# Kernel tuning notes

Measured on AMD Instinct MI355X. Metric: run time of the kernel, lower is better.

## Reference

```python
import jax, jax.numpy as jnp
import numpy as np
from jax import lax

# Conv3d(in_dim, in_dim, kernel=(1,3,3), padding=(0,1,1)) == per-time-slice 3x3 conv mixing channels

def _conv3d(x, w, b):
    # x: [B, C, T, W, H], w: [O, I, 1, 3, 3], b: [O]
    y = lax.conv_general_dilated(
        x, w,
        window_strides=(1, 1, 1),
        padding=[(0, 0), (1, 1), (1, 1)],
        dimension_numbers=("NCDHW", "OIDHW", "NCDHW"),
    )
    return y + b[None, :, None, None, None]


def setup_inputs() -> dict:
    key = jax.random.key(0)
    ks = jax.random.split(key, 8)
    B, C, T, W, H = 8, 64, 16, 64, 64
    fan = C * 1 * 3 * 3
    bound = 1.0 / np.sqrt(fan)  # torch Conv3d default init range
    x = jax.random.normal(ks[0], (B, C, T, W, H), dtype=jnp.float32)
    wq = jax.random.uniform(ks[1], (C, C, 1, 3, 3), jnp.float32, -bound, bound)
    wk = jax.random.uniform(ks[2], (C, C, 1, 3, 3), jnp.float32, -bound, bound)
    wv = jax.random.uniform(ks[3], (C, C, 1, 3, 3), jnp.float32, -bound, bound)
    bq = jax.random.uniform(ks[4], (C,), jnp.float32, -bound, bound)
    bk = jax.random.uniform(ks[5], (C,), jnp.float32, -bound, bound)
    bv = jax.random.uniform(ks[6], (C,), jnp.float32, -bound, bound)
    # torch init is gamma=0 (identity output); use nonzero so reference exercises the full path
    gamma = jax.random.normal(ks[7], (1,), dtype=jnp.float32) * 0.1
    return {"x": x, "wq": wq, "wk": wk, "wv": wv,
            "bq": bq, "bk": bk, "bv": bv, "gamma": gamma}


def reference(x, wq, wk, wv, bq, bk, bv, gamma):
    B, C, T, W, H = x.shape
    WH = W * H
    q = _conv3d(x, wq, bq).reshape(B, C, T, WH)
    k = _conv3d(x, wk, bk).reshape(B, C, T, WH)
    v = _conv3d(x, wv, bv).reshape(B, C, T, WH)
    # Original: (q[...,:,None] @ k[...,None,:]) @ v[...,:,None]  -> rank-1 energy, no softmax.
    # Exact reassociation: out_i = q_i * sum_j(k_j * v_j), avoiding the [WH, WH] matrix.
    s = jnp.sum(k * v, axis=-1, keepdims=True)  # [B, C, T, 1]
    out = (q * s).reshape(B, C, T, W, H)
    return gamma[0] * out + x
```

## Files before the change

kernel.cpp:

```cpp
#include <hip/hip_runtime.h>
#include <hip/hip_bf16.h>
#include <stdint.h>

typedef __attribute__((ext_vector_type(8))) short bf16x8;
typedef __attribute__((ext_vector_type(4))) float f32x4v;
typedef __attribute__((ext_vector_type(16))) float f32x16;

#define CH_STRIDE 65536
#define ROW_B 8448
#define SLICE_B 557568

__device__ __forceinline__ uint16_t f2bf(float f) {
  uint32_t u = __builtin_bit_cast(uint32_t, f);
  u = (u + 0x7FFFu + ((u >> 16) & 1u)) >> 16;
  return (uint16_t)u;
}
__device__ __forceinline__ float bf2f(uint32_t b) {
  return __builtin_bit_cast(float, b << 16);
}
__device__ __forceinline__ uint16_t cvt_bf(float f) {
  return __builtin_bit_cast(uint16_t, __float2bfloat16(f));
}

#define MFMA32(a, b, c) __builtin_amdgcn_mfma_f32_32x32x16_bf16(a, b, c, 0, 0, 0)
#define LGKM0 asm volatile("s_waitcnt lgkmcnt(0)" ::: "memory")
#define BAR __builtin_amdgcn_s_barrier()
#define SCHED0 __builtin_amdgcn_sched_barrier(0)

#define LDSX6  (6 * 8 * 66 * 16)
#define LDSX10 (10 * 8 * 66 * 16)

__device__ __forceinline__ bf16x8 ldx(const uint8_t* ldsx, int row, int oct, int ci) {
  return *(const bf16x8*)(ldsx + (uint32_t)((row * 8 + oct) * 66 + ci) * 16u);
}

__device__ __forceinline__ bf16x8 ldw_kv(const uint8_t* ldsw, int oct, int rowloc) {
  return *(const bf16x8*)(ldsw + (uint32_t)(oct * 128 + rowloc) * 16u);
}
__device__ __forceinline__ bf16x8 ldw_q(const uint8_t* ldsw, int oct, int row) {
  return *(const bf16x8*)(ldsw + (uint32_t)(oct * 64 + row) * 16u);
}
__device__ __forceinline__ void ldw_g_q(bf16x8* r, const uint16_t* wq, int tap, int tid) {
  #pragma unroll
  for (int k = 0; k < 2; ++k)
    r[k] = *(const bf16x8*)(wq + ((size_t)tap * 512 + tid + k * 256) * 8);
}
__device__ __forceinline__ void stw_q(uint8_t* ldsw, const bf16x8* r, int tid) {
  #pragma unroll
  for (int k = 0; k < 2; ++k)
    *(bf16x8*)(ldsw + (uint32_t)(tid + k * 256) * 16u) = r[k];
}

__global__ void prep_weights(const float* __restrict__ wq, const float* __restrict__ wk,
                             const float* __restrict__ wv, uint16_t* __restrict__ wout) {
  int i = blockIdx.x * 256 + threadIdx.x;
  if (i >= 110592) return;
  if (i < 36864) {
    int tap = i >> 12, oct = (i >> 9) & 7, row = (i >> 3) & 63, j = i & 7;
    wout[i] = f2bf(wq[(row * 64 + oct * 8 + j) * 9 + tap]);
  } else {
    int m = i - 36864;
    int tap = m >> 13, oct = (m >> 10) & 7, rl = (m >> 3) & 127, j = m & 7;
    const float* src = (rl < 64) ? wk : wv;
    wout[i] = f2bf(src[((rl & 63) * 64 + oct * 8 + j) * 9 + tap]);
  }
}

__global__ __launch_bounds__(256, 4) void transpose_x(const float* __restrict__ x,
                                                      uint8_t* __restrict__ xT) {
  __shared__ uint8_t lds[4 * 8 * 66 * 16];
  const int tid = threadIdx.x;
  const int bid = blockIdx.x;
  const int gg = bid % 17, slice = bid / 17;
  const int b = slice >> 4, t = slice & 15;
  const int r0 = gg * 4;
  const int nrow = (gg == 16) ? 2 : 4;
  const float* xs = x + ((size_t)b * 1024 + t) * 4096;

  if (tid < nrow * 16) {
    int row = tid >> 4, rem = tid & 15;
    int oct = rem >> 1, side = rem & 1;
    bf16x8 z = {};
    *(bf16x8*)(lds + (uint32_t)((row * 8 + oct) * 66 + side * 65) * 16u) = z;
  }
  #pragma unroll
  for (int k = 0; k < 2; ++k) {
    int u = tid + k * 256;
    if (u < nrow * 128) {
      int row = u >> 7, oct = (u >> 4) & 7, g = u & 15;
      int w = r0 + row - 1;
      uint32_t base = (uint32_t)((row * 8 + oct) * 66 + 4 * g + 1) * 16u;
      if ((unsigned)w < 64u) {
        const float* p = xs + (size_t)(oct * 8) * CH_STRIDE + w * 64 + 4 * g;
        f32x4v v[8];
        #pragma unroll
        for (int j = 0; j < 8; ++j) v[j] = *(const f32x4v*)(p + (size_t)j * CH_STRIDE);
        #pragma unroll
        for (int c = 0; c < 4; ++c) {
          bf16x8 frag;
          #pragma unroll
          for (int q = 0; q < 4; ++q) {
            frag[2 * q]     = (short)cvt_bf(v[2 * q][c]);
            frag[2 * q + 1] = (short)cvt_bf(v[2 * q + 1][c]);
          }
          *(bf16x8*)(lds + base + (uint32_t)c * 16u) = frag;
        }
      } else {
        bf16x8 z = {};
        #pragma unroll
        for (int c = 0; c < 4; ++c)
          *(bf16x8*)(lds + base + (uint32_t)c * 16u) = z;
      }
    }
  }
  __syncthreads();
  uint8_t* dst = xT + (size_t)slice * SLICE_B + (size_t)r0 * 528 * 16;
  for (int i = tid; i < nrow * 528; i += 256)
    *(bf16x8*)(dst + (uint32_t)i * 16u) = *(const bf16x8*)(lds + (uint32_t)i * 16u);
}

__global__ __launch_bounds__(1024, 4) void kv_s_kernel(
    const uint8_t* __restrict__ xT, const uint16_t* __restrict__ wkv,
    const float* __restrict__ bk, const float* __restrict__ bv,
    float* __restrict__ s_out) {
  extern __shared__ uint8_t lds[];
  uint8_t* ldsx = lds;
  uint8_t* ldswA = lds + LDSX10;
  uint8_t* ldswB = lds + LDSX10 + 16384;
  const int tid = threadIdx.x;
  const int l = tid & 63;
  const int wid = tid >> 6;
  const int ng = wid & 7, mg = wid >> 3;
  int bid = (int)(blockIdx.x & 7) * 128 + (int)(blockIdx.x >> 3);
  const int rg = bid & 7, slice = bid >> 3;
  const int b = slice >> 4, t = slice & 15;
  const int w0 = rg * 8;
  const int lm = l & 31, lh = l >> 5;

  const uint8_t* gx = xT + (size_t)slice * SLICE_B + (size_t)w0 * ROW_B;
  #pragma unroll
  for (int k = 0; k < 6; ++k) {
    int idx = tid + k * 1024;
    if (idx < 5280)
      *(bf16x8*)(ldsx + (uint32_t)idx * 16u) = *(const bf16x8*)(gx + (uint32_t)idx * 16u);
  }
  bf16x8 r_pref;
  r_pref = *(const bf16x8*)(wkv + (size_t)tid * 8);
  *(bf16x8*)(ldswA + (uint32_t)tid * 16u) = r_pref;
  r_pref = *(const bf16x8*)(wkv + ((size_t)1024 + tid) * 8);
  SCHED0; LGKM0; BAR; SCHED0;

  f32x16 accK[2], accV[2];
  #pragma unroll
  for (int nt = 0; nt < 2; ++nt)
    #pragma unroll
    for (int q = 0; q < 16; ++q) { accK[nt][q] = 0.f; accV[nt][q] = 0.f; }

  #pragma unroll
  for (int tap = 0; tap < 9; ++tap) {
    const int dy = tap / 3, dx = tap % 3;
    const uint8_t* bufc = (tap & 1) ? ldswB : ldswA;
    uint8_t* bufn = (tap & 1) ? ldswA : ldswB;
    int oct0 = lh;
    bf16x8 aK = ldw_kv(bufc, oct0, mg * 32 + lm);
    bf16x8 aV = ldw_kv(bufc, oct0, 64 + mg * 32 + lm);
    bf16x8 b0 = ldx(ldsx, ng + dy, oct0, lm + dx);
    bf16x8 b1 = ldx(ldsx, ng + dy, oct0, 32 + lm + dx);
    if (tap < 8) {
      *(bf16x8*)(bufn + (uint32_t)tid * 16u) = r_pref;
      if (tap < 7)
        r_pref = *(const bf16x8*)(wkv + ((size_t)(tap + 2) * 1024 + tid) * 8);
    }
    __builtin_amdgcn_s_setprio(1);
    accK[0] = MFMA32(aK, b0, accK[0]);
    accK[1] = MFMA32(aK, b1, accK[1]);
    accV[0] = MFMA32(aV, b0, accV[0]);
    accV[1] = MFMA32(aV, b1, accV[1]);
    #pragma unroll
    for (int s = 1; s < 4; ++s) {
      int oct = s * 2 + lh;
      aK = ldw_kv(bufc, oct, mg * 32 + lm);
      aV = ldw_kv(bufc, oct, 64 + mg * 32 + lm);
      b0 = ldx(ldsx, ng + dy, oct, lm + dx);
      b1 = ldx(ldsx, ng + dy, oct, 32 + lm + dx);
      accK[0] = MFMA32(aK, b0, accK[0]);
      accK[1] = MFMA32(aK, b1, accK[1]);
      accV[0] = MFMA32(aV, b0, accV[0]);
      accV[1] = MFMA32(aV, b1, accV[1]);
    }
    __builtin_amdgcn_s_setprio(0);
    SCHED0; LGKM0; BAR; SCHED0;
  }

  __syncthreads();
  float* red = (float*)lds;
  #pragma unroll
  for (int q = 0; q < 16; ++q) {
    int cl = (q & 3) + 8 * (q >> 2) + 4 * lh;
    int c = mg * 32 + cl;
    float bkc = bk[c], bvc = bv[c];
    float p = (accK[0][q] + bkc) * (accV[0][q] + bvc)
            + (accK[1][q] + bkc) * (accV[1][q] + bvc);
    red[c * 261 + ng * 32 + lm] = p;
  }
  __syncthreads();
  if (tid < 64) {
    const float* rp = red + tid * 261;
    f32x4v a4 = {0.f, 0.f, 0.f, 0.f};
    #pragma unroll
    for (int j = 0; j < 64; ++j) a4 += *(const f32x4v*)(rp + j * 4);
    atomicAdd(s_out + (b * 16 + t) * 64 + tid, a4[0] + a4[1] + a4[2] + a4[3]);
  }
}

__global__ __launch_bounds__(256, 2) void q_out_kernel(
    const uint8_t* __restrict__ xT, const uint16_t* __restrict__ wq,
    const float* __restrict__ bq, const float* __restrict__ s_in,
    const float* __restrict__ gamma, float* __restrict__ out) {
  extern __shared__ uint8_t lds[];
  uint8_t* ldsx = lds;
  uint8_t* ldsw = lds + LDSX6;
  const int tid = threadIdx.x;
  const int l = tid & 63, ng = tid >> 6;
  int bid = (int)(blockIdx.x & 7) * 256 + (int)(blockIdx.x >> 3);
  const int rg = bid & 15, slice = bid >> 4;
  const int b = slice >> 4, t = slice & 15;
  const int w0 = rg * 4;
  const int lm = l & 31, lh = l >> 5;

  const uint8_t* gx = xT + (size_t)slice * SLICE_B + (size_t)w0 * ROW_B;
  #pragma unroll
  for (int k = 0; k < 13; ++k) {
    int idx = tid + k * 256;
    if (idx < 3168)
      *(bf16x8*)(ldsx + (uint32_t)idx * 16u) = *(const bf16x8*)(gx + (uint32_t)idx * 16u);
  }
  bf16x8 r[2];
  ldw_g_q(r, wq, 0, tid);
  stw_q(ldsw, r, tid);
  ldw_g_q(r, wq, 1, tid);
  SCHED0; LGKM0; BAR; SCHED0;

  f32x16 acc[2][2];
  #pragma unroll
  for (int mt = 0; mt < 2; ++mt)
    #pragma unroll
    for (int nt = 0; nt < 2; ++nt)
      #pragma unroll
      for (int q = 0; q < 16; ++q) acc[mt][nt][q] = 0.f;

  #pragma unroll
  for (int tap = 0; tap < 9; ++tap) {
    const int dy = tap / 3, dx = tap % 3;
    __builtin_amdgcn_s_setprio(1);
    #pragma unroll
    for (int s = 0; s < 4; ++s) {
      int oct = s * 2 + lh;
      bf16x8 a0 = ldw_q(ldsw, oct, lm);
      bf16x8 a1 = ldw_q(ldsw, oct, 32 + lm);
      bf16x8 b0 = ldx(ldsx, ng + dy, oct, lm + dx);
      bf16x8 b1 = ldx(ldsx, ng + dy, oct, 32 + lm + dx);
      acc[0][0] = MFMA32(a0, b0, acc[0][0]);
      acc[0][1] = MFMA32(a0, b1, acc[0][1]);
      acc[1][0] = MFMA32(a1, b0, acc[1][0]);
      acc[1][1] = MFMA32(a1, b1, acc[1][1]);
    }
    __builtin_amdgcn_s_setprio(0);
    if (tap < 8) {
      SCHED0; BAR;
      stw_q(ldsw, r, tid);
      if (tap < 7) ldw_g_q(r, wq, tap + 2, tid);
      SCHED0; LGKM0; BAR; SCHED0;
    }
  }

  float g = gamma[0];
  const float* sb = s_in + (b * 16 + t) * 64;
  int w = w0 + ng;
  #pragma unroll
  for (int mt = 0; mt < 2; ++mt) {
    #pragma unroll
    for (int q = 0; q < 16; ++q) {
      int cl = (q & 3) + 8 * (q >> 2) + 4 * lh;
      int c  = mt * 32 + cl;
      float qb = bq[c], sc = sb[c];
      #pragma unroll
      for (int nt = 0; nt < 2; ++nt) {
        int h = nt * 32 + lm;
        uint32_t xb = (uint32_t)(((ng + 1) * 8 + (c >> 3)) * 66 + (h + 1)) * 16u
                    + (uint32_t)(c & 7) * 2u;
        float xv = bf2f(*(const uint16_t*)(ldsx + xb));
        size_t idx = ((size_t)(b * 64 + c) * 16 + t) * 4096 + (size_t)w * 64 + h;
        out[idx] = g * (acc[mt][nt][q] + qb) * sc + xv;
      }
    }
  }
}

extern "C" void kernel_launch(void* const* d_in, const int* in_sizes, int n_in,
                              void* d_out, int out_size, void* d_ws, size_t ws_size,
                              hipStream_t stream) {
  const float* x   = (const float*)d_in[0];
  const float* wq  = (const float*)d_in[1];
  const float* wk  = (const float*)d_in[2];
  const float* wv  = (const float*)d_in[3];
  const float* bq  = (const float*)d_in[4];
  const float* bk  = (const float*)d_in[5];
  const float* bv  = (const float*)d_in[6];
  const float* gam = (const float*)d_in[7];

  uint16_t* wbf = (uint16_t*)d_ws;
  float* sbuf   = (float*)((uint8_t*)d_ws + 221184);
  uint8_t* xT   = (uint8_t*)d_ws + 1048576;
  if (ws_size < (size_t)1048576 + 128 * (size_t)SLICE_B) return;

  hipMemsetAsync(sbuf, 0, 8 * 16 * 64 * sizeof(float), stream);
  prep_weights<<<(110592 + 255) / 256, 256, 0, stream>>>(wq, wk, wv, wbf);
  transpose_x<<<128 * 17, 256, 0, stream>>>(x, xT);
  kv_s_kernel<<<1024, 1024, LDSX10 + 32768, stream>>>(xT, wbf + 36864, bk, bv, sbuf);
  q_out_kernel<<<2048, 256, LDSX6 + 8192, stream>>>(xT, wbf, bq, sbuf, gam, (float*)d_out);
}
```

Baseline: 181.8 us.

## Use direct global-to-LDS loads and double-buffer Q weights; drop LDS staging in transpose

Replaces the register-staged global→LDS copies of x tiles and weights in the kv and q kernels with global_load_lds DMA-style loads, so data skips VGPRs. The q kernel gets double-buffered weight tiles, which removes one barrier per tap. The transpose kernel now writes bf16 fragments straight to global memory instead of staging them through shared memory. Each tap now waits on vmcnt(0), which exposes global load latency in exchange for fewer instructions, and the doubled LDS in the q kernel may reduce occupancy.

```diff
diff --git a/kernel.cpp b/kernel.cpp
--- a/kernel.cpp
+++ b/kernel.cpp
@@ -23,32 +23,27 @@
 }
 
 #define MFMA32(a, b, c) __builtin_amdgcn_mfma_f32_32x32x16_bf16(a, b, c, 0, 0, 0)
-#define LGKM0 asm volatile("s_waitcnt lgkmcnt(0)" ::: "memory")
+#define WAIT0 asm volatile("s_waitcnt vmcnt(0) lgkmcnt(0)" ::: "memory")
 #define BAR __builtin_amdgcn_s_barrier()
 #define SCHED0 __builtin_amdgcn_sched_barrier(0)
 
 #define LDSX6  (6 * 8 * 66 * 16)
 #define LDSX10 (10 * 8 * 66 * 16)
 
+__device__ __forceinline__ void gld16(const void* g, void* l) {
+  __builtin_amdgcn_global_load_lds(
+      (const __attribute__((address_space(1))) uint32_t*)g,
+      (__attribute__((address_space(3))) uint32_t*)l, 16, 0, 0);
+}
+
 __device__ __forceinline__ bf16x8 ldx(const uint8_t* ldsx, int row, int oct, int ci) {
   return *(const bf16x8*)(ldsx + (uint32_t)((row * 8 + oct) * 66 + ci) * 16u);
 }
-
 __device__ __forceinline__ bf16x8 ldw_kv(const uint8_t* ldsw, int oct, int rowloc) {
   return *(const bf16x8*)(ldsw + (uint32_t)(oct * 128 + rowloc) * 16u);
 }
 __device__ __forceinline__ bf16x8 ldw_q(const uint8_t* ldsw, int oct, int row) {
   return *(const bf16x8*)(ldsw + (uint32_t)(oct * 64 + row) * 16u);
-}
-__device__ __forceinline__ void ldw_g_q(bf16x8* r, const uint16_t* wq, int tap, int tid) {
-  #pragma unroll
-  for (int k = 0; k < 2; ++k)
-    r[k] = *(const bf16x8*)(wq + ((size_t)tap * 512 + tid + k * 256) * 8);
-}
-__device__ __forceinline__ void stw_q(uint8_t* ldsw, const bf16x8* r, int tid) {
-  #pragma unroll
-  for (int k = 0; k < 2; ++k)
-    *(bf16x8*)(ldsw + (uint32_t)(tid + k * 256) * 16u) = r[k];
 }
 
 __global__ void prep_weights(const float* __restrict__ wq, const float* __restrict__ wk,
@@ -68,7 +63,6 @@
 
 __global__ __launch_bounds__(256, 4) void transpose_x(const float* __restrict__ x,
                                                       uint8_t* __restrict__ xT) {
-  __shared__ uint8_t lds[4 * 8 * 66 * 16];
   const int tid = threadIdx.x;
   const int bid = blockIdx.x;
   const int gg = bid % 17, slice = bid / 17;
@@ -76,12 +70,13 @@
   const int r0 = gg * 4;
   const int nrow = (gg == 16) ? 2 : 4;
   const float* xs = x + ((size_t)b * 1024 + t) * 4096;
+  uint8_t* dst = xT + (size_t)slice * SLICE_B + (size_t)r0 * ROW_B;
 
   if (tid < nrow * 16) {
     int row = tid >> 4, rem = tid & 15;
     int oct = rem >> 1, side = rem & 1;
     bf16x8 z = {};
-    *(bf16x8*)(lds + (uint32_t)((row * 8 + oct) * 66 + side * 65) * 16u) = z;
+    *(bf16x8*)(dst + (uint32_t)((row * 8 + oct) * 66 + side * 65) * 16u) = z;
   }
   #pragma unroll
   for (int k = 0; k < 2; ++k) {
@@ -89,7 +84,7 @@
     if (u < nrow * 128) {
       int row = u >> 7, oct = (u >> 4) & 7, g = u & 15;
       int w = r0 + row - 1;
-      uint32_t base = (uint32_t)((row * 8 + oct) * 66 + 4 * g + 1) * 16u;
+      uint8_t* base = dst + (uint32_t)((row * 8 + oct) * 66 + 4 * g + 1) * 16u;
       if ((unsigned)w < 64u) {
         const float* p = xs + (size_t)(oct * 8) * CH_STRIDE + w * 64 + 4 * g;
         f32x4v v[8];
@@ -103,20 +98,15 @@
             frag[2 * q]     = (short)cvt_bf(v[2 * q][c]);
             frag[2 * q + 1] = (short)cvt_bf(v[2 * q + 1][c]);
           }
-          *(bf16x8*)(lds + base + (uint32_t)c * 16u) = frag;
+          *(bf16x8*)(base + (uint32_t)c * 16u) = frag;
         }
       } else {
         bf16x8 z = {};
         #pragma unroll
-        for (int c = 0; c < 4; ++c)
-          *(bf16x8*)(lds + base + (uint32_t)c * 16u) = z;
+        for (int c = 0; c < 4; ++c) *(bf16x8*)(base + (uint32_t)c * 16u) = z;
       }
     }
   }
-  __syncthreads();
-  uint8_t* dst = xT + (size_t)slice * SLICE_B + (size_t)r0 * 528 * 16;
-  for (int i = tid; i < nrow * 528; i += 256)
-    *(bf16x8*)(dst + (uint32_t)i * 16u) = *(const bf16x8*)(lds + (uint32_t)i * 16u);
 }
 
 __global__ __launch_bounds__(1024, 4) void kv_s_kernel(
@@ -141,14 +131,10 @@
   #pragma unroll
   for (int k = 0; k < 6; ++k) {
     int idx = tid + k * 1024;
-    if (idx < 5280)
-      *(bf16x8*)(ldsx + (uint32_t)idx * 16u) = *(const bf16x8*)(gx + (uint32_t)idx * 16u);
-  }
-  bf16x8 r_pref;
-  r_pref = *(const bf16x8*)(wkv + (size_t)tid * 8);
-  *(bf16x8*)(ldswA + (uint32_t)tid * 16u) = r_pref;
-  r_pref = *(const bf16x8*)(wkv + ((size_t)1024 + tid) * 8);
-  SCHED0; LGKM0; BAR; SCHED0;
+    if (idx < 5280) gld16(gx + (uint32_t)idx * 16u, ldsx + (uint32_t)idx * 16u);
+  }
+  gld16(wkv + (size_t)tid * 8, ldswA + (uint32_t)tid * 16u);
+  SCHED0; WAIT0; BAR; SCHED0;
 
   f32x16 accK[2], accV[2];
   #pragma unroll
@@ -161,35 +147,23 @@
     const int dy = tap / 3, dx = tap % 3;
     const uint8_t* bufc = (tap & 1) ? ldswB : ldswA;
     uint8_t* bufn = (tap & 1) ? ldswA : ldswB;
-    int oct0 = lh;
-    bf16x8 aK = ldw_kv(bufc, oct0, mg * 32 + lm);
-    bf16x8 aV = ldw_kv(bufc, oct0, 64 + mg * 32 + lm);
-    bf16x8 b0 = ldx(ldsx, ng + dy, oct0, lm + dx);
-    bf16x8 b1 = ldx(ldsx, ng + dy, oct0, 32 + lm + dx);
-    if (tap < 8) {
-      *(bf16x8*)(bufn + (uint32_t)tid * 16u) = r_pref;
-      if (tap < 7)
-        r_pref = *(const bf16x8*)(wkv + ((size_t)(tap + 2) * 1024 + tid) * 8);
-    }
+    if (tap < 8)
+      gld16(wkv + ((size_t)(tap + 1) * 1024 + tid) * 8, bufn + (uint32_t)tid * 16u);
     __builtin_amdgcn_s_setprio(1);
-    accK[0] = MFMA32(aK, b0, accK[0]);
-    accK[1] = MFMA32(aK, b1, accK[1]);
-    accV[0] = MFMA32(aV, b0, accV[0]);
-    accV[1] = MFMA32(aV, b1, accV[1]);
-    #pragma unroll
-    for (int s = 1; s < 4; ++s) {
+    #pragma unroll
+    for (int s = 0; s < 4; ++s) {
       int oct = s * 2 + lh;
-      aK = ldw_kv(bufc, oct, mg * 32 + lm);
-      aV = ldw_kv(bufc, oct, 64 + mg * 32 + lm);
-      b0 = ldx(ldsx, ng + dy, oct, lm + dx);
-      b1 = ldx(ldsx, ng + dy, oct, 32 + lm + dx);
+      bf16x8 aK = ldw_kv(bufc, oct, mg * 32 + lm);
+      bf16x8 aV = ldw_kv(bufc, oct, 64 + mg * 32 + lm);
+      bf16x8 b0 = ldx(ldsx, ng + dy, oct, lm + dx);
+      bf16x8 b1 = ldx(ldsx, ng + dy, oct, 32 + lm + dx);
       accK[0] = MFMA32(aK, b0, accK[0]);
       accK[1] = MFMA32(aK, b1, accK[1]);
       accV[0] = MFMA32(aV, b0, accV[0]);
       accV[1] = MFMA32(aV, b1, accV[1]);
     }
     __builtin_amdgcn_s_setprio(0);
-    SCHED0; LGKM0; BAR; SCHED0;
+    SCHED0; WAIT0; BAR; SCHED0;
   }
 
   __syncthreads();
@@ -219,7 +193,8 @@
     const float* __restrict__ gamma, float* __restrict__ out) {
   extern __shared__ uint8_t lds[];
   uint8_t* ldsx = lds;
-  uint8_t* ldsw = lds + LDSX6;
+  uint8_t* ldswA = lds + LDSX6;
+  uint8_t* ldswB = lds + LDSX6 + 8192;
   const int tid = threadIdx.x;
   const int l = tid & 63, ng = tid >> 6;
   int bid = (int)(blockIdx.x & 7) * 256 + (int)(blockIdx.x >> 3);
@@ -232,14 +207,12 @@
   #pragma unroll
   for (int k = 0; k < 13; ++k) {
     int idx = tid + k * 256;
-    if (idx < 3168)
-      *(bf16x8*)(ldsx + (uint32_t)idx * 16u) = *(const bf16x8*)(gx + (uint32_t)idx * 16u);
-  }
-  bf16x8 r[2];
-  ldw_g_q(r, wq, 0, tid);
-  stw_q(ldsw, r, tid);
-  ldw_g_q(r, wq, 1, tid);
-  SCHED0; LGKM0; BAR; SCHED0;
+    if (idx < 3168) gld16(gx + (uint32_t)idx * 16u, ldsx + (uint32_t)idx * 16u);
+  }
+  #pragma unroll
+  for (int k = 0; k < 2; ++k)
+    gld16(wq + (size_t)(tid + k * 256) * 8, ldswA + (uint32_t)(tid + k * 256) * 16u);
+  SCHED0; WAIT0; BAR; SCHED0;
 
   f32x16 acc[2][2];
   #pragma unroll
@@ -252,12 +225,20 @@
   #pragma unroll
   for (int tap = 0; tap < 9; ++tap) {
     const int dy = tap / 3, dx = tap % 3;
+    const uint8_t* bufc = (tap & 1) ? ldswB : ldswA;
+    uint8_t* bufn = (tap & 1) ? ldswA : ldswB;
+    if (tap < 8) {
+      #pragma unroll
+      for (int k = 0; k < 2; ++k)
+        gld16(wq + ((size_t)(tap + 1) * 512 + tid + k * 256) * 8,
+              bufn + (uint32_t)(tid + k * 256) * 16u);
+    }
     __builtin_amdgcn_s_setprio(1);
     #pragma unroll
     for (int s = 0; s < 4; ++s) {
       int oct = s * 2 + lh;
-      bf16x8 a0 = ldw_q(ldsw, oct, lm);
-      bf16x8 a1 = ldw_q(ldsw, oct, 32 + lm);
+      bf16x8 a0 = ldw_q(bufc, oct, lm);
+      bf16x8 a1 = ldw_q(bufc, oct, 32 + lm);
       bf16x8 b0 = ldx(ldsx, ng + dy, oct, lm + dx);
       bf16x8 b1 = ldx(ldsx, ng + dy, oct, 32 + lm + dx);
       acc[0][0] = MFMA32(a0, b0, acc[0][0]);
@@ -266,12 +247,7 @@
       acc[1][1] = MFMA32(a1, b1, acc[1][1]);
     }
     __builtin_amdgcn_s_setprio(0);
-    if (tap < 8) {
-      SCHED0; BAR;
-      stw_q(ldsw, r, tid);
-      if (tap < 7) ldw_g_q(r, wq, tap + 2, tid);
-      SCHED0; LGKM0; BAR; SCHED0;
-    }
+    SCHED0; WAIT0; BAR; SCHED0;
   }
 
   float g = gamma[0];
@@ -318,5 +294,5 @@
   prep_weights<<<(110592 + 255) / 256, 256, 0, stream>>>(wq, wk, wv, wbf);
   transpose_x<<<128 * 17, 256, 0, stream>>>(x, xT);
   kv_s_kernel<<<1024, 1024, LDSX10 + 32768, stream>>>(xT, wbf + 36864, bk, bv, sbuf);
-  q_out_kernel<<<2048, 256, LDSX6 + 8192, stream>>>(xT, wbf, bq, sbuf, gam, (float*)d_out);
-}
+  q_out_kernel<<<2048, 256, LDSX6 + 16384, stream>>>(xT, wbf, bq, sbuf, gam, (float*)d_out);
+}
```

New measurement: 180.2 us. Within noise of the previous version (-0.9%).
